# Kernel tuning notes

Measured on AMD Instinct MI355X. Metric: run time of the kernel, lower is better.

The kernel has to match this reference:

```python
import jax, jax.numpy as jnp
import numpy as np

D = 128  # node_dim
H = 256  # edge_hidden_dim
B, N = 32, 128
EPS = 1e-5


def _glorot(key, shape):
    fan_in = shape[0]
    bound = 1.0 / np.sqrt(fan_in)
    return jax.random.uniform(key, shape, jnp.float32, -bound, bound)


def setup_inputs() -> dict:
    key = jax.random.key(0)
    ks = jax.random.split(key, 12)
    nodes = jax.random.normal(ks[0], (B, N, D), jnp.float32)
    node_mask = (jax.random.uniform(ks[1], (B, N)) < 0.9).astype(jnp.float32)
    return {
        "nodes": nodes,
        "node_mask": node_mask,
        # LayerNorm params
        "ln_g": jnp.ones((D,), jnp.float32),
        "ln_b": jnp.zeros((D,), jnp.float32),
        # msg_mlp: Linear(2D->H), ReLU, Linear(H->D), ReLU  (weights stored [in,out])
        "mw1": _glorot(ks[2], (2 * D, H)),
        "mb1": _glorot(ks[3], (2 * D, H))[0],
        "mw2": _glorot(ks[4], (H, D)),
        "mb2": _glorot(ks[5], (H, D))[0],
        # upd_mlp: Linear(2D->H), ReLU, Linear(H->D)
        "uw1": _glorot(ks[6], (2 * D, H)),
        "ub1": _glorot(ks[7], (2 * D, H))[0],
        "uw2": _glorot(ks[8], (H, D)),
        "ub2": _glorot(ks[9], (H, D))[0],
    }


def _layernorm(x, g, b):
    mu = jnp.mean(x, axis=-1, keepdims=True)
    var = jnp.var(x, axis=-1, keepdims=True)
    return (x - mu) * jax.lax.rsqrt(var + EPS) * g + b


def reference(nodes, node_mask, ln_g, ln_b, mw1, mb1, mw2, mb2, uw1, ub1, uw2, ub2):
    mask = node_mask[..., None]                      # [B,N,1]
    x = _layernorm(nodes, ln_g, ln_b) * mask          # [B,N,D]
    # cat([x_i, x_j]) @ mw1 == x_i @ mw1[:D] + x_j @ mw1[D:]  (avoids 2D concat)
    xi_p = jnp.einsum('bnd,dh->bnh', x, mw1[:D])      # receiver projection
    xj_p = jnp.einsum('bnd,dh->bnh', x, mw1[D:])      # sender projection
    h = jax.nn.relu(xi_p[:, :, None, :] + xj_p[:, None, :, :] + mb1)  # [B,N,N,H]
    msgs = jax.nn.relu(jnp.einsum('bijh,hd->bijd', h, mw2) + mb2)     # [B,N,N,D]
    msgs = msgs * mask[:, None]                       # mask senders j
    agg = jnp.sum(msgs, axis=2)                       # [B,N,D]
    u = jax.nn.relu(jnp.einsum('bnd,dh->bnh', nodes, uw1[:D])
                    + jnp.einsum('bnd,dh->bnh', agg, uw1[D:]) + ub1)
    new_nodes = nodes + jnp.einsum('bnh,hd->bnd', u, uw2) + ub2
    return new_nodes * mask
```

## Files before the change

kernel.cpp:

```cpp
#include <hip/hip_runtime.h>
#include <hip/hip_bf16.h>

#define D 128
#define H 256
#define NB 32
#define NN 128

typedef __attribute__((ext_vector_type(8))) _Float16 f16x8;
typedef __attribute__((ext_vector_type(4))) float f32x4;
typedef __attribute__((ext_vector_type(16))) float f32x16;
typedef __attribute__((ext_vector_type(4))) unsigned int uint4v;

__device__ __forceinline__ unsigned short to_f16u(float f) {
  _Float16 h = (_Float16)f;
  return __builtin_bit_cast(unsigned short, h);
}

__device__ __forceinline__ unsigned cvt_pk_f16(float lo, float hi) {
  unsigned d;
  asm("v_cvt_pkrtz_f16_f32 %0, %1, %2" : "=v"(d) : "v"(lo), "v"(hi));
  return d;
}

__device__ __forceinline__ unsigned pk_add_f16(unsigned a, unsigned b) {
  unsigned d;
  asm("v_pk_add_f16 %0, %1, %2" : "=v"(d) : "v"(a), "v"(b));
  return d;
}

__device__ __forceinline__ unsigned pk_relu(unsigned x) {
  unsigned d;
  asm("v_pk_max_i16 %0, %1, %2" : "=v"(d) : "v"(x), "v"(0u));
  return d;
}

__global__ __launch_bounds__(512) void k_repack(
    const float* __restrict__ mw1, const float* __restrict__ uw1,
    const float* __restrict__ uw2, const float* __restrict__ mw2,
    unsigned short* __restrict__ w1f, unsigned short* __restrict__ w3f,
    unsigned short* __restrict__ w4f, unsigned short* __restrict__ bw2) {
  const int gt = blockIdx.x * 512 + threadIdx.x;
  const int tile = gt >> 6, l = gt & 63;
  const int lg = l >> 4, l15 = l & 15;
  if (tile < 128) {
    const int ks = tile >> 5, ntg = tile & 31;
#pragma unroll
    for (int e = 0; e < 8; ++e) {
      int k = ks * 32 + lg * 8 + e;
      int col = ntg * 16 + l15;
      float v = (col < 256) ? mw1[k * 256 + col] : mw1[(128 + k) * 256 + (col - 256)];
      w1f[(size_t)(tile * 64 + l) * 8 + e] = to_f16u(v);
    }
  } else if (tile < 256) {
    const int t = tile - 128, ks = t >> 4, ntg = t & 15;
#pragma unroll
    for (int e = 0; e < 8; ++e) {
      int k = ks * 32 + lg * 8 + e;
      w3f[(size_t)(t * 64 + l) * 8 + e] = to_f16u(uw1[k * 256 + ntg * 16 + l15]);
    }
  } else if (tile < 320) {
    const int t = tile - 256, ks = t >> 3, ntg = t & 7;
#pragma unroll
    for (int e = 0; e < 8; ++e) {
      int k = ks * 32 + lg * 8 + e;
      w4f[(size_t)(t * 64 + l) * 8 + e] = to_f16u(uw2[k * 128 + ntg * 16 + l15]);
    }
  } else {
    const int t = tile - 320;
    const int st = t >> 2, ntile = t & 3;
    const int lh = l >> 5, l31 = l & 31;
#pragma unroll
    for (int e = 0; e < 8; ++e) {
      int k = st * 16 + lh * 8 + e;
      bw2[(size_t)(t * 64 + l) * 8 + e] = to_f16u(mw2[k * 128 + ntile * 32 + l31]);
    }
  }
}

__global__ __launch_bounds__(256) void k_ln_proj(
    const float* __restrict__ nodes, const float* __restrict__ node_mask,
    const float* __restrict__ ln_g, const float* __restrict__ ln_b,
    const unsigned short* __restrict__ w1f,
    float* __restrict__ xi_p, unsigned short* __restrict__ xjh) {
  const int row0 = blockIdx.x * 16;
  const int half = blockIdx.y;
  const int tid = threadIdx.x;
  __shared__ unsigned short xh[16 * 128];

  {
    const int r = tid >> 4, l16 = tid & 15, d0 = l16 * 8;
    float4 v0 = *(const float4*)(nodes + (size_t)(row0 + r) * D + d0);
    float4 v1 = *(const float4*)(nodes + (size_t)(row0 + r) * D + d0 + 4);
    float s1 = v0.x + v0.y + v0.z + v0.w + v1.x + v1.y + v1.z + v1.w;
    float s2 = v0.x * v0.x + v0.y * v0.y + v0.z * v0.z + v0.w * v0.w +
               v1.x * v1.x + v1.y * v1.y + v1.z * v1.z + v1.w * v1.w;
#pragma unroll
    for (int off = 1; off < 16; off <<= 1) {
      s1 += __shfl_xor(s1, off);
      s2 += __shfl_xor(s2, off);
    }
    float mu = s1 * (1.0f / 128.0f);
    float var = s2 * (1.0f / 128.0f) - mu * mu;
    float rsig = rsqrtf(var + 1e-5f);
    float m = node_mask[row0 + r];
    float4 g0 = *(const float4*)(ln_g + d0), g1 = *(const float4*)(ln_g + d0 + 4);
    float4 b0 = *(const float4*)(ln_b + d0), b1 = *(const float4*)(ln_b + d0 + 4);
    float x0 = ((v0.x - mu) * rsig * g0.x + b0.x) * m;
    float x1 = ((v0.y - mu) * rsig * g0.y + b0.y) * m;
    float x2 = ((v0.z - mu) * rsig * g0.z + b0.z) * m;
    float x3 = ((v0.w - mu) * rsig * g0.w + b0.w) * m;
    float x4 = ((v1.x - mu) * rsig * g1.x + b1.x) * m;
    float x5 = ((v1.y - mu) * rsig * g1.y + b1.y) * m;
    float x6 = ((v1.z - mu) * rsig * g1.z + b1.z) * m;
    float x7 = ((v1.w - mu) * rsig * g1.w + b1.w) * m;
    uint4v u;
    u[0] = cvt_pk_f16(x0, x1); u[1] = cvt_pk_f16(x2, x3);
    u[2] = cvt_pk_f16(x4, x5); u[3] = cvt_pk_f16(x6, x7);
    const int g = l16 ^ (r & 7);
    *(uint4v*)(&xh[r * 128 + g * 8]) = u;
  }
  __syncthreads();

  const int w = tid >> 6, l = tid & 63;
  const int lg = l >> 4, l15 = l & 15;
  f32x4 acc[4];
#pragma unroll
  for (int nt = 0; nt < 4; ++nt) acc[nt] = (f32x4){0.f, 0.f, 0.f, 0.f};

#pragma unroll
  for (int ks = 0; ks < 4; ++ks) {
    const int g = (ks * 4 + lg) ^ (l15 & 7);
    f16x8 a = *(const f16x8*)(&xh[l15 * 128 + g * 8]);
#pragma unroll
    for (int nt = 0; nt < 4; ++nt) {
      const int tile = ks * 32 + half * 16 + w * 4 + nt;
      f16x8 bf = *(const f16x8*)(w1f + (size_t)(tile * 64 + l) * 8);
      acc[nt] = __builtin_amdgcn_mfma_f32_16x16x32_f16(a, bf, acc[nt], 0, 0, 0);
    }
  }

  if (half == 0) {
#pragma unroll
    for (int nt = 0; nt < 4; ++nt)
#pragma unroll
      for (int r = 0; r < 4; ++r)
        xi_p[(size_t)(row0 + lg * 4 + r) * H + w * 64 + nt * 16 + l15] = acc[nt][r];
  } else {
#pragma unroll
    for (int nt = 0; nt < 4; ++nt)
#pragma unroll
      for (int r = 0; r < 4; ++r)
        xjh[(size_t)(row0 + lg * 4 + r) * H + w * 64 + nt * 16 + l15] = to_f16u(acc[nt][r]);
  }
}

__global__ __launch_bounds__(1024, 4) void k_msgs(
    const float* __restrict__ xi_p, const unsigned short* __restrict__ xjh,
    const unsigned short* __restrict__ bw2g, const float* __restrict__ mb1,
    const float* __restrict__ mb2, const float* __restrict__ node_mask,
    float* __restrict__ agg) {
  const int blk = blockIdx.x;
  const int b = blk >> 3;
  const int iq0 = (blk & 7) * 4;
  const int tid = threadIdx.x;
  const int w = tid >> 6, l = tid & 63;
  const int ipair = w >> 3;
  const int jslab = (w & 7) >> 1;
  const int nh = w & 1;
  const int jbase = jslab * 32;
  const int l31 = l & 31, lh = l >> 5;

  __shared__ unsigned short bw2s[32768];
  __shared__ unsigned short xjs[32768];
  __shared__ unsigned cs2[4][128];
  __shared__ float mb2s[128], maskS[128];
  __shared__ float waveAgg[16][2][64];

  {
    const uint4v* src = (const uint4v*)bw2g;
    uint4v* dst = (uint4v*)bw2s;
#pragma unroll
    for (int c = 0; c < 4; ++c) dst[c * 1024 + tid] = src[c * 1024 + tid];
  }
  {
    const int jj = tid & 127;
    const int qq = tid >> 7;
    const int js = jj >> 5, j31 = jj & 31;
    const unsigned short* grow = xjh + (size_t)(b * NN + jj) * H;
    uint4v* dst = (uint4v*)xjs;
#pragma unroll
    for (int r = 0; r < 4; ++r) {
      const int c = qq * 4 + r;
      const int st = c >> 1, lhh = c & 1;
      dst[((js * 16 + st) * 2 + lhh) * 32 + j31] =
          *(const uint4v*)(grow + c * 8);
    }
  }
  if (tid < 128) { mb2s[tid] = mb2[tid]; maskS[tid] = node_mask[b * NN + tid]; }

  const uint4v* bfrag = (const uint4v*)bw2s;
  const uint4v* xfrag = (const uint4v*)xjs;

  for (int t = 0; t < 4; ++t) {
    const int i0 = (iq0 + t) * 4;
    __syncthreads();
    if (tid < 512) {
      int ii = tid >> 7, p = tid & 127;
      float2 xi2 = *(const float2*)(xi_p + (size_t)(b * NN + i0 + ii) * H + 2 * p);
      float2 mbv = *(const float2*)(mb1 + 2 * p);
      cs2[ii][p] = cvt_pk_f16(xi2.x + mbv.x, xi2.y + mbv.y);
    }
    __syncthreads();

    f32x16 acc[2][2];
#pragma unroll
    for (int ii = 0; ii < 2; ++ii)
#pragma unroll
      for (int nt = 0; nt < 2; ++nt)
#pragma unroll
        for (int r = 0; r < 16; ++r) acc[ii][nt][r] = 0.f;

#pragma unroll
    for (int st = 0; st < 16; ++st) {
      const int kb = st * 16 + lh * 8;
      uint4v xu = xfrag[((jslab * 16 + st) * 2 + lh) * 32 + l31];
      uint4v cc0 = *(const uint4v*)(&cs2[ipair * 2 + 0][kb >> 1]);
      uint4v cc1 = *(const uint4v*)(&cs2[ipair * 2 + 1][kb >> 1]);
      uint4v a0, a1;
#pragma unroll
      for (int p = 0; p < 4; ++p) {
        a0[p] = pk_relu(pk_add_f16(xu[p], cc0[p]));
        a1[p] = pk_relu(pk_add_f16(xu[p], cc1[p]));
      }
      f16x8 af0 = __builtin_bit_cast(f16x8, a0);
      f16x8 af1 = __builtin_bit_cast(f16x8, a1);
#pragma unroll
      for (int nt = 0; nt < 2; ++nt) {
        f16x8 bf = __builtin_bit_cast(f16x8, bfrag[(st * 4 + nh * 2 + nt) * 64 + l]);
        acc[0][nt] = __builtin_amdgcn_mfma_f32_32x32x16_f16(af0, bf, acc[0][nt], 0, 0, 0);
        acc[1][nt] = __builtin_amdgcn_mfma_f32_32x32x16_f16(af1, bf, acc[1][nt], 0, 0, 0);
      }
    }

#pragma unroll
    for (int ii = 0; ii < 2; ++ii)
#pragma unroll
      for (int nt = 0; nt < 2; ++nt) {
        const float bias = mb2s[nh * 64 + nt * 32 + l31];
        float s = 0.f;
#pragma unroll
        for (int reg = 0; reg < 16; ++reg) {
          const int j = jbase + 4 * lh + (reg & 3) + 8 * (reg >> 2);
          s = fmaf(fmaxf(acc[ii][nt][reg] + bias, 0.f), maskS[j], s);
        }
        s += __shfl_xor(s, 32);
        if (l < 32) waveAgg[w][ii][nt * 32 + l31] = s;
      }
    __syncthreads();
    if (tid < 512) {
      const int ii4 = tid >> 7, col = tid & 127;
      const int ipq = ii4 >> 1, iwi = ii4 & 1;
      const int nh2 = col >> 6, c6 = col & 63;
      agg[(size_t)(b * NN + i0 + ii4) * D + col] =
          waveAgg[ipq * 8 + 0 + nh2][iwi][c6] + waveAgg[ipq * 8 + 2 + nh2][iwi][c6] +
          waveAgg[ipq * 8 + 4 + nh2][iwi][c6] + waveAgg[ipq * 8 + 6 + nh2][iwi][c6];
    }
  }
}

__global__ __launch_bounds__(256) void k_upd(
    const float* __restrict__ nodes, const float* __restrict__ agg,
    const unsigned short* __restrict__ w3f, const float* __restrict__ ub1,
    const unsigned short* __restrict__ w4f, const float* __restrict__ ub2,
    const float* __restrict__ node_mask, float* __restrict__ out) {
  const int row0 = blockIdx.x * 16;
  const int tid = threadIdx.x;
  __shared__ unsigned short ah[16 * 256];
  __shared__ unsigned short uh[16 * 256];
  __shared__ float ns[16][128];
  __shared__ float msk[16];

  {
    const int r = tid >> 4, l16 = tid & 15, d0 = l16 * 8;
    float4 n0 = *(const float4*)(nodes + (size_t)(row0 + r) * D + d0);
    float4 n1 = *(const float4*)(nodes + (size_t)(row0 + r) * D + d0 + 4);
    *(float4*)(&ns[r][d0]) = n0;
    *(float4*)(&ns[r][d0 + 4]) = n1;
    uint4v u;
    u[0] = cvt_pk_f16(n0.x, n0.y); u[1] = cvt_pk_f16(n0.z, n0.w);
    u[2] = cvt_pk_f16(n1.x, n1.y); u[3] = cvt_pk_f16(n1.z, n1.w);
    int g = l16 ^ (r & 7);
    *(uint4v*)(&ah[r * 256 + g * 8]) = u;
    float4 a0 = *(const float4*)(agg + (size_t)(row0 + r) * D + d0);
    float4 a1 = *(const float4*)(agg + (size_t)(row0 + r) * D + d0 + 4);
    u[0] = cvt_pk_f16(a0.x, a0.y); u[1] = cvt_pk_f16(a0.z, a0.w);
    u[2] = cvt_pk_f16(a1.x, a1.y); u[3] = cvt_pk_f16(a1.z, a1.w);
    g = (16 + l16) ^ (r & 7);
    *(uint4v*)(&ah[r * 256 + g * 8]) = u;
    if (tid < 16) msk[tid] = node_mask[row0 + tid];
  }
  __syncthreads();

  const int w = tid >> 6, l = tid & 63;
  const int lg = l >> 4, l15 = l & 15;

  f32x4 acc[4];
#pragma unroll
  for (int nt = 0; nt < 4; ++nt) acc[nt] = (f32x4){0.f, 0.f, 0.f, 0.f};
#pragma unroll
  for (int ks = 0; ks < 8; ++ks) {
    const int g = (ks * 4 + lg) ^ (l15 & 7);
    f16x8 a = *(const f16x8*)(&ah[l15 * 256 + g * 8]);
#pragma unroll
    for (int nt = 0; nt < 4; ++nt) {
      const int tile = ks * 16 + w * 4 + nt;
      f16x8 bf = *(const f16x8*)(w3f + (size_t)(tile * 64 + l) * 8);
      acc[nt] = __builtin_amdgcn_mfma_f32_16x16x32_f16(a, bf, acc[nt], 0, 0, 0);
    }
  }
#pragma unroll
  for (int nt = 0; nt < 4; ++nt) {
    const int col = w * 64 + nt * 16 + l15;
    const float bias = ub1[col];
#pragma unroll
    for (int r = 0; r < 4; ++r) {
      const int row = lg * 4 + r;
      const int g = (col >> 3) ^ (row & 7);
      uh[row * 256 + g * 8 + (col & 7)] = to_f16u(fmaxf(acc[nt][r] + bias, 0.f));
    }
  }
  __syncthreads();

  f32x4 acc2[2];
  acc2[0] = (f32x4){0.f, 0.f, 0.f, 0.f};
  acc2[1] = (f32x4){0.f, 0.f, 0.f, 0.f};
#pragma unroll
  for (int ks = 0; ks < 8; ++ks) {
    const int g = (ks * 4 + lg) ^ (l15 & 7);
    f16x8 a = *(const f16x8*)(&uh[l15 * 256 + g * 8]);
#pragma unroll
    for (int nt = 0; nt < 2; ++nt) {
      const int tile = ks * 8 + w * 2 + nt;
      f16x8 bf = *(const f16x8*)(w4f + (size_t)(tile * 64 + l) * 8);
      acc2[nt] = __builtin_amdgcn_mfma_f32_16x16x32_f16(a, bf, acc2[nt], 0, 0, 0);
    }
  }
#pragma unroll
  for (int nt = 0; nt < 2; ++nt) {
    const int col = w * 32 + nt * 16 + l15;
    const float ub2v = ub2[col];
#pragma unroll
    for (int r = 0; r < 4; ++r) {
      const int row = lg * 4 + r;
      out[(size_t)(row0 + row) * D + col] =
          (ns[row][col] + acc2[nt][r] + ub2v) * msk[row];
    }
  }
}

extern "C" void kernel_launch(void* const* d_in, const int* in_sizes, int n_in,
                              void* d_out, int out_size, void* d_ws, size_t ws_size,
                              hipStream_t stream) {
  (void)in_sizes; (void)n_in; (void)out_size; (void)ws_size;
  const float* nodes     = (const float*)d_in[0];
  const float* node_mask = (const float*)d_in[1];
  const float* ln_g      = (const float*)d_in[2];
  const float* ln_b      = (const float*)d_in[3];
  const float* mw1       = (const float*)d_in[4];
  const float* mb1       = (const float*)d_in[5];
  const float* mw2       = (const float*)d_in[6];
  const float* mb2       = (const float*)d_in[7];
  const float* uw1       = (const float*)d_in[8];
  const float* ub1       = (const float*)d_in[9];
  const float* uw2       = (const float*)d_in[10];
  const float* ub2       = (const float*)d_in[11];
  float* out = (float*)d_out;

  char* ws = (char*)d_ws;
  float*          xi_p = (float*)(ws);
  unsigned short* xjh  = (unsigned short*)(ws + ((size_t)4 << 20));
  float*          agg  = (float*)(ws + ((size_t)6 << 20));
  unsigned short* bw2  = (unsigned short*)(ws + ((size_t)8 << 20));
  unsigned short* w1f  = (unsigned short*)(ws + ((size_t)8 << 20) + (64 << 10));
  unsigned short* w3f  = (unsigned short*)(ws + ((size_t)8 << 20) + (192 << 10));
  unsigned short* w4f  = (unsigned short*)(ws + ((size_t)8 << 20) + (320 << 10));

  k_repack<<<48, 512, 0, stream>>>(mw1, uw1, uw2, mw2, w1f, w3f, w4f, bw2);
  k_ln_proj<<<dim3(256, 2), 256, 0, stream>>>(nodes, node_mask, ln_g, ln_b, w1f, xi_p, xjh);
  k_msgs<<<256, 1024, 0, stream>>>(xi_p, xjh, bw2, mb1, mb2, node_mask, agg);
  k_upd<<<256, 256, 0, stream>>>(nodes, agg, w3f, ub1, w4f, ub2, node_mask, out);
}
```

Before: 57.25 us.

## Fuse update MLP into message kernel, keeping aggregates in shared memory

Moves the update-MLP stage into the end of the message kernel, so each block writes its 16 aggregated rows to LDS and immediately runs both update GEMMs. This removes the separate k_upd launch and the global write/read of agg. It enlarges LDS usage to about 147 KB by aliasing buffers and adds a serialized tail phase with fewer active waves per block.

After: 54.70 us. 4.4% less time.

```diff
diff --git a/kernel.cpp b/kernel.cpp
--- a/kernel.cpp
+++ b/kernel.cpp
@@ -158,10 +158,13 @@
     const float* __restrict__ xi_p, const unsigned short* __restrict__ xjh,
     const unsigned short* __restrict__ bw2g, const float* __restrict__ mb1,
     const float* __restrict__ mb2, const float* __restrict__ node_mask,
-    float* __restrict__ agg) {
+    const float* __restrict__ nodes, const unsigned short* __restrict__ w3f,
+    const float* __restrict__ ub1, const unsigned short* __restrict__ w4f,
+    const float* __restrict__ ub2, float* __restrict__ out) {
   const int blk = blockIdx.x;
   const int b = blk >> 3;
   const int iq0 = (blk & 7) * 4;
+  const int i16 = (blk & 7) * 16;
   const int tid = threadIdx.x;
   const int w = tid >> 6, l = tid & 63;
   const int ipair = w >> 3;
@@ -169,12 +172,20 @@
   const int nh = w & 1;
   const int jbase = jslab * 32;
   const int l31 = l & 31, lh = l >> 5;
-
-  __shared__ unsigned short bw2s[32768];
-  __shared__ unsigned short xjs[32768];
-  __shared__ unsigned cs2[4][128];
-  __shared__ float mb2s[128], maskS[128];
-  __shared__ float waveAgg[16][2][64];
+  const int lg = (l >> 4) & 3, l15 = l & 15;
+
+  __shared__ __align__(16) char smem[150528];
+  unsigned short* bw2s = (unsigned short*)smem;
+  unsigned short* xjs  = (unsigned short*)(smem + 65536);
+  unsigned* cs2        = (unsigned*)(smem + 131072);
+  float* mb2s          = (float*)(smem + 133120);
+  float* maskS         = (float*)(smem + 133632);
+  float* waveAgg       = (float*)(smem + 134144);
+  float* aggL          = (float*)(smem + 142336);
+  unsigned short* ah   = (unsigned short*)(smem + 65536);
+  unsigned short* uh   = (unsigned short*)(smem + 73728);
+  float* nsf           = (float*)(smem + 81920);
+  float* msk           = (float*)(smem + 90112);
 
   {
     const uint4v* src = (const uint4v*)bw2g;
@@ -208,7 +219,7 @@
       int ii = tid >> 7, p = tid & 127;
       float2 xi2 = *(const float2*)(xi_p + (size_t)(b * NN + i0 + ii) * H + 2 * p);
       float2 mbv = *(const float2*)(mb1 + 2 * p);
-      cs2[ii][p] = cvt_pk_f16(xi2.x + mbv.x, xi2.y + mbv.y);
+      cs2[ii * 128 + p] = cvt_pk_f16(xi2.x + mbv.x, xi2.y + mbv.y);
     }
     __syncthreads();
 
@@ -224,8 +235,8 @@
     for (int st = 0; st < 16; ++st) {
       const int kb = st * 16 + lh * 8;
       uint4v xu = xfrag[((jslab * 16 + st) * 2 + lh) * 32 + l31];
-      uint4v cc0 = *(const uint4v*)(&cs2[ipair * 2 + 0][kb >> 1]);
-      uint4v cc1 = *(const uint4v*)(&cs2[ipair * 2 + 1][kb >> 1]);
+      uint4v cc0 = *(const uint4v*)(&cs2[(ipair * 2 + 0) * 128 + (kb >> 1)]);
+      uint4v cc1 = *(const uint4v*)(&cs2[(ipair * 2 + 1) * 128 + (kb >> 1)]);
       uint4v a0, a1;
 #pragma unroll
       for (int p = 0; p < 4; ++p) {
@@ -254,106 +265,80 @@
           s = fmaf(fmaxf(acc[ii][nt][reg] + bias, 0.f), maskS[j], s);
         }
         s += __shfl_xor(s, 32);
-        if (l < 32) waveAgg[w][ii][nt * 32 + l31] = s;
+        if (l < 32) waveAgg[((w * 2) + ii) * 64 + nt * 32 + l31] = s;
       }
     __syncthreads();
     if (tid < 512) {
       const int ii4 = tid >> 7, col = tid & 127;
       const int ipq = ii4 >> 1, iwi = ii4 & 1;
       const int nh2 = col >> 6, c6 = col & 63;
-      agg[(size_t)(b * NN + i0 + ii4) * D + col] =
-          waveAgg[ipq * 8 + 0 + nh2][iwi][c6] + waveAgg[ipq * 8 + 2 + nh2][iwi][c6] +
-          waveAgg[ipq * 8 + 4 + nh2][iwi][c6] + waveAgg[ipq * 8 + 6 + nh2][iwi][c6];
-    }
-  }
-}
-
-__global__ __launch_bounds__(256) void k_upd(
-    const float* __restrict__ nodes, const float* __restrict__ agg,
-    const unsigned short* __restrict__ w3f, const float* __restrict__ ub1,
-    const unsigned short* __restrict__ w4f, const float* __restrict__ ub2,
-    const float* __restrict__ node_mask, float* __restrict__ out) {
-  const int row0 = blockIdx.x * 16;
-  const int tid = threadIdx.x;
-  __shared__ unsigned short ah[16 * 256];
-  __shared__ unsigned short uh[16 * 256];
-  __shared__ float ns[16][128];
-  __shared__ float msk[16];
-
-  {
+      aggL[(t * 4 + ii4) * 128 + col] =
+          waveAgg[((ipq * 8 + 0 + nh2) * 2 + iwi) * 64 + c6] +
+          waveAgg[((ipq * 8 + 2 + nh2) * 2 + iwi) * 64 + c6] +
+          waveAgg[((ipq * 8 + 4 + nh2) * 2 + iwi) * 64 + c6] +
+          waveAgg[((ipq * 8 + 6 + nh2) * 2 + iwi) * 64 + c6];
+    }
+  }
+  __syncthreads();
+
+  if (tid < 256) {
     const int r = tid >> 4, l16 = tid & 15, d0 = l16 * 8;
-    float4 n0 = *(const float4*)(nodes + (size_t)(row0 + r) * D + d0);
-    float4 n1 = *(const float4*)(nodes + (size_t)(row0 + r) * D + d0 + 4);
-    *(float4*)(&ns[r][d0]) = n0;
-    *(float4*)(&ns[r][d0 + 4]) = n1;
+    const size_t grow = (size_t)(b * NN + i16 + r) * D;
+    float4 n0 = *(const float4*)(nodes + grow + d0);
+    float4 n1 = *(const float4*)(nodes + grow + d0 + 4);
+    *(float4*)(&nsf[r * 128 + d0]) = n0;
+    *(float4*)(&nsf[r * 128 + d0 + 4]) = n1;
     uint4v u;
     u[0] = cvt_pk_f16(n0.x, n0.y); u[1] = cvt_pk_f16(n0.z, n0.w);
     u[2] = cvt_pk_f16(n1.x, n1.y); u[3] = cvt_pk_f16(n1.z, n1.w);
     int g = l16 ^ (r & 7);
     *(uint4v*)(&ah[r * 256 + g * 8]) = u;
-    float4 a0 = *(const float4*)(agg + (size_t)(row0 + r) * D + d0);
-    float4 a1 = *(const float4*)(agg + (size_t)(row0 + r) * D + d0 + 4);
+    float4 a0 = *(const float4*)(&aggL[r * 128 + d0]);
+    float4 a1 = *(const float4*)(&aggL[r * 128 + d0 + 4]);
     u[0] = cvt_pk_f16(a0.x, a0.y); u[1] = cvt_pk_f16(a0.z, a0.w);
     u[2] = cvt_pk_f16(a1.x, a1.y); u[3] = cvt_pk_f16(a1.z, a1.w);
     g = (16 + l16) ^ (r & 7);
     *(uint4v*)(&ah[r * 256 + g * 8]) = u;
-    if (tid < 16) msk[tid] = node_mask[row0 + tid];
+    if (tid < 16) msk[tid] = node_mask[b * NN + i16 + tid];
   }
   __syncthreads();
 
-  const int w = tid >> 6, l = tid & 63;
-  const int lg = l >> 4, l15 = l & 15;
-
-  f32x4 acc[4];
-#pragma unroll
-  for (int nt = 0; nt < 4; ++nt) acc[nt] = (f32x4){0.f, 0.f, 0.f, 0.f};
-#pragma unroll
-  for (int ks = 0; ks < 8; ++ks) {
-    const int g = (ks * 4 + lg) ^ (l15 & 7);
-    f16x8 a = *(const f16x8*)(&ah[l15 * 256 + g * 8]);
-#pragma unroll
-    for (int nt = 0; nt < 4; ++nt) {
-      const int tile = ks * 16 + w * 4 + nt;
-      f16x8 bf = *(const f16x8*)(w3f + (size_t)(tile * 64 + l) * 8);
-      acc[nt] = __builtin_amdgcn_mfma_f32_16x16x32_f16(a, bf, acc[nt], 0, 0, 0);
-    }
-  }
-#pragma unroll
-  for (int nt = 0; nt < 4; ++nt) {
-    const int col = w * 64 + nt * 16 + l15;
+  {
+    f32x4 acc3 = (f32x4){0.f, 0.f, 0.f, 0.f};
+#pragma unroll
+    for (int ks = 0; ks < 8; ++ks) {
+      const int g = (ks * 4 + lg) ^ (l15 & 7);
+      f16x8 a = *(const f16x8*)(&ah[l15 * 256 + g * 8]);
+      f16x8 bf = *(const f16x8*)(w3f + (size_t)((ks * 16 + w) * 64 + l) * 8);
+      acc3 = __builtin_amdgcn_mfma_f32_16x16x32_f16(a, bf, acc3, 0, 0, 0);
+    }
+    const int col = w * 16 + l15;
     const float bias = ub1[col];
 #pragma unroll
     for (int r = 0; r < 4; ++r) {
       const int row = lg * 4 + r;
-      const int g = (col >> 3) ^ (row & 7);
-      uh[row * 256 + g * 8 + (col & 7)] = to_f16u(fmaxf(acc[nt][r] + bias, 0.f));
+      const int g2 = (col >> 3) ^ (row & 7);
+      uh[row * 256 + g2 * 8 + (col & 7)] = to_f16u(fmaxf(acc3[r] + bias, 0.f));
     }
   }
   __syncthreads();
 
-  f32x4 acc2[2];
-  acc2[0] = (f32x4){0.f, 0.f, 0.f, 0.f};
-  acc2[1] = (f32x4){0.f, 0.f, 0.f, 0.f};
-#pragma unroll
-  for (int ks = 0; ks < 8; ++ks) {
-    const int g = (ks * 4 + lg) ^ (l15 & 7);
-    f16x8 a = *(const f16x8*)(&uh[l15 * 256 + g * 8]);
-#pragma unroll
-    for (int nt = 0; nt < 2; ++nt) {
-      const int tile = ks * 8 + w * 2 + nt;
-      f16x8 bf = *(const f16x8*)(w4f + (size_t)(tile * 64 + l) * 8);
-      acc2[nt] = __builtin_amdgcn_mfma_f32_16x16x32_f16(a, bf, acc2[nt], 0, 0, 0);
-    }
-  }
-#pragma unroll
-  for (int nt = 0; nt < 2; ++nt) {
-    const int col = w * 32 + nt * 16 + l15;
+  if (w < 8) {
+    f32x4 acc4 = (f32x4){0.f, 0.f, 0.f, 0.f};
+#pragma unroll
+    for (int ks = 0; ks < 8; ++ks) {
+      const int g = (ks * 4 + lg) ^ (l15 & 7);
+      f16x8 a = *(const f16x8*)(&uh[l15 * 256 + g * 8]);
+      f16x8 bf = *(const f16x8*)(w4f + (size_t)((ks * 8 + w) * 64 + l) * 8);
+      acc4 = __builtin_amdgcn_mfma_f32_16x16x32_f16(a, bf, acc4, 0, 0, 0);
+    }
+    const int col = w * 16 + l15;
     const float ub2v = ub2[col];
 #pragma unroll
     for (int r = 0; r < 4; ++r) {
       const int row = lg * 4 + r;
-      out[(size_t)(row0 + row) * D + col] =
-          (ns[row][col] + acc2[nt][r] + ub2v) * msk[row];
+      out[(size_t)(b * NN + i16 + row) * D + col] =
+          (nsf[row * 128 + col] + acc4[r] + ub2v) * msk[row];
     }
   }
 }
@@ -379,14 +364,13 @@
   char* ws = (char*)d_ws;
   float*          xi_p = (float*)(ws);
   unsigned short* xjh  = (unsigned short*)(ws + ((size_t)4 << 20));
-  float*          agg  = (float*)(ws + ((size_t)6 << 20));
-  unsigned short* bw2  = (unsigned short*)(ws + ((size_t)8 << 20));
-  unsigned short* w1f  = (unsigned short*)(ws + ((size_t)8 << 20) + (64 << 10));
-  unsigned short* w3f  = (unsigned short*)(ws + ((size_t)8 << 20) + (192 << 10));
-  unsigned short* w4f  = (unsigned short*)(ws + ((size_t)8 << 20) + (320 << 10));
+  unsigned short* bw2  = (unsigned short*)(ws + ((size_t)6 << 20));
+  unsigned short* w1f  = (unsigned short*)(ws + ((size_t)6 << 20) + (64 << 10));
+  unsigned short* w3f  = (unsigned short*)(ws + ((size_t)6 << 20) + (192 << 10));
+  unsigned short* w4f  = (unsigned short*)(ws + ((size_t)6 << 20) + (320 << 10));
 
   k_repack<<<48, 512, 0, stream>>>(mw1, uw1, uw2, mw2, w1f, w3f, w4f, bw2);
   k_ln_proj<<<dim3(256, 2), 256, 0, stream>>>(nodes, node_mask, ln_g, ln_b, w1f, xi_p, xjh);
-  k_msgs<<<256, 1024, 0, stream>>>(xi_p, xjh, bw2, mb1, mb2, node_mask, agg);
-  k_upd<<<256, 256, 0, stream>>>(nodes, agg, w3f, ub1, w4f, ub2, node_mask, out);
-}
+  k_msgs<<<256, 1024, 0, stream>>>(xi_p, xjh, bw2, mb1, mb2, node_mask,
+                                   nodes, w3f, ub1, w4f, ub2, out);
+}
```
